# Performance work log

Measured on AMD Instinct MI355X. Metric: run time of the kernel, lower is better.

Reference implementation:

```python
import jax, jax.numpy as jnp
import numpy as np

H_SIZE = 2048
NUM_K_HEADS = 16
NUM_V_HEADS = 32
DK = 128
DV = 128
KEY_DIM = NUM_K_HEADS * DK        # 2048
VALUE_DIM = NUM_V_HEADS * DV      # 4096
CONV_DIM = 2 * KEY_DIM + VALUE_DIM  # 8192
KERNEL = 4
EPS = 1e-6
B, S = 2, 2048


def setup_inputs() -> dict:
    key = jax.random.key(0)
    ks = jax.random.split(key, 8)
    w = lambda k, shape, s: jax.random.normal(k, shape, jnp.float32) * s
    return {
        "hidden_states": jax.random.normal(ks[0], (B, S, H_SIZE), jnp.float32),
        "w_qkv": w(ks[1], (H_SIZE, CONV_DIM), 0.02),
        "w_z": w(ks[2], (H_SIZE, VALUE_DIM), 0.02),
        "w_b": w(ks[3], (H_SIZE, NUM_V_HEADS), 0.02),
        "w_a": w(ks[4], (H_SIZE, NUM_V_HEADS), 0.02),
        "conv_w": w(ks[5], (CONV_DIM, KERNEL), 0.2),
        "dt_bias": jnp.ones((NUM_V_HEADS,), jnp.float32),
        "A_log": jnp.zeros((NUM_V_HEADS,), jnp.float32),
        "norm_gamma": jnp.ones((DV,), jnp.float32),
        "w_out": w(ks[6], (VALUE_DIM, H_SIZE), 0.02),
    }


def _l2norm(x, eps=1e-6):
    return x * jax.lax.rsqrt(jnp.sum(x * x, axis=-1, keepdims=True) + eps)


def _causal_conv(x, w):
    # depthwise causal conv1d; x: (B,S,C), w: (C,K)
    K = w.shape[-1]
    Sq = x.shape[1]
    xp = jnp.pad(x, ((0, 0), (K - 1, 0), (0, 0)))
    out = xp[:, 0:Sq, :] * w[None, None, :, 0]
    for j in range(1, K):  # tiny fixed kernel loop (K=4)
        out = out + xp[:, j:j + Sq, :] * w[None, None, :, j]
    return out


def _forward(hidden_states, w_qkv, w_z, w_b, w_a, conv_w, dt_bias, A_log,
             norm_gamma, w_out):
    Bq, Sq, _ = hidden_states.shape
    mixed = hidden_states @ w_qkv                       # (B,S,CONV_DIM)
    z = (hidden_states @ w_z).reshape(Bq, Sq, NUM_V_HEADS, DV)
    b = hidden_states @ w_b                             # (B,S,Hv)
    a = hidden_states @ w_a                             # (B,S,Hv)
    mixed = jax.nn.silu(_causal_conv(mixed, conv_w))
    q, k, v = jnp.split(mixed, [KEY_DIM, 2 * KEY_DIM], axis=-1)
    q = q.reshape(Bq, Sq, NUM_K_HEADS, DK)
    k = k.reshape(Bq, Sq, NUM_K_HEADS, DK)
    v = v.reshape(Bq, Sq, NUM_V_HEADS, DV)
    nrep = NUM_V_HEADS // NUM_K_HEADS
    q = jnp.repeat(q, nrep, axis=2)                     # GQA expand -> Hv heads
    k = jnp.repeat(k, nrep, axis=2)
    beta = jax.nn.sigmoid(b)                            # write gate
    g = -jnp.exp(A_log)[None, None, :] * jax.nn.softplus(a + dt_bias[None, None, :])

    # gated delta rule recurrence in float32 (matches reference)
    qf = _l2norm(q.astype(jnp.float32)) * (DK ** -0.5)
    kf = _l2norm(k.astype(jnp.float32))
    vf = v.astype(jnp.float32)
    gf = g.astype(jnp.float32)
    bf = beta.astype(jnp.float32)

    def step(state, xs):
        q_t, k_t, v_t, g_t, b_t = xs  # (B,H,dk),(B,H,dk),(B,H,dv),(B,H),(B,H)
        state = state * jnp.exp(g_t)[..., None, None]
        kv = jnp.einsum('bhk,bhkv->bhv', k_t, state)
        delta = (v_t - kv) * b_t[..., None]
        state = state + jnp.einsum('bhk,bhv->bhkv', k_t, delta)
        out = jnp.einsum('bhk,bhkv->bhv', q_t, state)
        return state, out

    mv = lambda x: jnp.moveaxis(x, 1, 0)  # (B,S,...) -> (S,B,...)
    xs = (mv(qf), mv(kf), mv(vf), mv(gf), mv(bf))
    state0 = jnp.zeros((Bq, NUM_V_HEADS, DK, DV), jnp.float32)
    _, outs = jax.lax.scan(step, state0, xs)            # (S,B,H,dv)
    o = jnp.moveaxis(outs, 0, 1)                        # (B,S,H,dv)

    # gated RMSNorm over head_v_dim: gate with silu(z), then rms-normalize
    o = o * jax.nn.silu(z.astype(jnp.float32))
    o = o * jax.lax.rsqrt(jnp.mean(o * o, axis=-1, keepdims=True) + EPS)
    o = o * norm_gamma
    o = o.reshape(Bq, Sq, VALUE_DIM).astype(hidden_states.dtype)
    return o @ w_out


def reference(hidden_states, w_qkv, w_z, w_b, w_a, conv_w, dt_bias, A_log,
              norm_gamma, w_out):
    return _forward(hidden_states, w_qkv, w_z, w_b, w_a, conv_w, dt_bias,
                    A_log, norm_gamma, w_out)
```

## Files before the change

### kernel.cpp

```cpp
#include <hip/hip_runtime.h>
#include <hip/hip_bf16.h>
#include <cstdint>


#define HSZ 2048
#define NUM_K_HEADS 16
#define NUM_V_HEADS 32
#define DKH 128
#define DVH 128
#define KEY_DIM 2048
#define VALUE_DIM 4096
#define CONV_DIM 8192
#define BB 2
#define SSEQ 2048
#define MM (BB * SSEQ)
#define CHUNK 64
#define NCHUNK (SSEQ / CHUNK)
#define DVB 16

typedef __hip_bfloat16 bf16;
typedef short short8 __attribute__((ext_vector_type(8)));
typedef float f32x4 __attribute__((ext_vector_type(4)));

__device__ __forceinline__ float bfu(ushort u) {
  union { float f; uint32_t i; } x;
  x.i = ((uint32_t)u) << 16;
  return x.f;
}
__device__ __forceinline__ ushort f2b(float f) {
  bf16 h = __float2bfloat16(f);
  return *reinterpret_cast<ushort*>(&h);
}

__device__ __forceinline__ void gload16(const void* g, const void* l) {
  __builtin_amdgcn_global_load_lds(
      (const __attribute__((address_space(1))) unsigned int*)g,
      (__attribute__((address_space(3))) unsigned int*)(const_cast<void*>(l)),
      16, 0, 0);
}

__device__ __forceinline__ int kidx(int r, int d) {
  return r * 128 + (((d >> 3) ^ (r & 7)) << 3) + (d & 7);
}
__device__ __forceinline__ int widx(int r, int d) {
  return r * 64 + (((d >> 3) ^ (r & 7)) << 3) + (d & 7);
}

__global__ __launch_bounds__(256) void cast_bf16_kernel(
    const float* __restrict__ in, ushort* __restrict__ out, int n4) {
  int i = blockIdx.x * 256 + threadIdx.x;
  if (i < n4) {
    float4 v = ((const float4*)in)[i];
    ushort4 u;
    u.x = f2b(v.x); u.y = f2b(v.y); u.z = f2b(v.z); u.w = f2b(v.w);
    ((ushort4*)out)[i] = u;
  }
}

__global__ __launch_bounds__(256) void transpose_cast(
    const float* __restrict__ W, ushort* __restrict__ WT, int K, int N) {
  __shared__ ushort tile[32][33];
  const int tx = threadIdx.x & 31, ty = threadIdx.x >> 5;
  const int n0 = blockIdx.x * 32, k0 = blockIdx.y * 32;
#pragma unroll
  for (int i = 0; i < 4; ++i)
    tile[ty + i * 8][tx] = f2b(W[(size_t)(k0 + ty + i * 8) * N + n0 + tx]);
  __syncthreads();
#pragma unroll
  for (int i = 0; i < 4; ++i)
    WT[(size_t)(n0 + ty + i * 8) * K + k0 + tx] = tile[tx][ty + i * 8];
}

__global__ __launch_bounds__(512) void gemm256_fused(
    const ushort* __restrict__ A, const ushort* __restrict__ BT,
    ushort* __restrict__ Cm, ushort* __restrict__ Cz, int M, int K) {
  __shared__ __align__(16) ushort smem[256 * 264];
  const int t = threadIdx.x;
  const int w = t >> 6, lane = t & 63;
  const int m0 = blockIdx.y * 256, n0 = blockIdx.x * 256;
  const int wm = (w >> 2) * 128, wn = (w & 3) * 64;
  const int fr = lane & 15, kb = lane >> 4;
  const int srow = t >> 3;
  const int scol = (t & 7) * 8;
  const int ssw = ((scol >> 3) ^ (srow & 7)) << 3;
  const int rsw = fr & 7;
  f32x4 acc[8][4] = {};
  const int nt = K / 64;

#define STAGE_TILE(tt, buf)                                                   \
  {                                                                           \
    const int k0_ = (tt)*64;                                                  \
    ushort* As_ = smem + (buf)*32768;                                         \
    ushort* Bs_ = As_ + 16384;                                                \
    _Pragma("unroll") for (int p = 0; p < 4; ++p) {                           \
      const int row_ = p * 64 + srow;                                         \
      gload16(&A[(size_t)(m0 + row_) * K + k0_ + ssw],                        \
              &As_[row_ * 64 + scol]);                                        \
    }                                                                         \
    _Pragma("unroll") for (int p = 0; p < 4; ++p) {                           \
      const int row_ = p * 64 + srow;                                         \
      gload16(&BT[(size_t)(n0 + row_) * K + k0_ + ssw],                       \
              &Bs_[row_ * 64 + scol]);                                        \
    }                                                                         \
  }

  STAGE_TILE(0, 0);
  STAGE_TILE(1, 1);

  for (int tt = 0; tt < nt; ++tt) {
    const int buf = tt & 1;
    const ushort* As = smem + buf * 32768;
    const ushort* Bs = As + 16384;
    if (tt + 1 < nt)
      asm volatile("s_waitcnt vmcnt(8)" ::: "memory");
    else
      asm volatile("s_waitcnt vmcnt(0)" ::: "memory");
    __builtin_amdgcn_sched_barrier(0);
    __builtin_amdgcn_s_barrier();
    __builtin_amdgcn_sched_barrier(0);
#pragma unroll
    for (int ks = 0; ks < 2; ++ks) {
      const int kg = ks * 4 + kb;
      const int ca = ((kg ^ rsw) << 3);
      short8 af[8], bf_[4];
#pragma unroll
      for (int mf = 0; mf < 8; ++mf)
        af[mf] = *(const short8*)&As[(wm + mf * 16 + fr) * 64 + ca];
#pragma unroll
      for (int nf = 0; nf < 4; ++nf)
        bf_[nf] = *(const short8*)&Bs[(wn + nf * 16 + fr) * 64 + ca];
#pragma unroll
      for (int mf = 0; mf < 8; ++mf)
#pragma unroll
        for (int nf = 0; nf < 4; ++nf)
          acc[mf][nf] = __builtin_amdgcn_mfma_f32_16x16x32_bf16(
              af[mf], bf_[nf], acc[mf][nf], 0, 0, 0);
    }
    __builtin_amdgcn_sched_barrier(0);
    __builtin_amdgcn_s_barrier();
    __builtin_amdgcn_sched_barrier(0);
    if (tt + 2 < nt) STAGE_TILE(tt + 2, buf);
  }
#undef STAGE_TILE

  const int crow = wm + (lane >> 4) * 4;
  const int ccol = wn + fr;
#pragma unroll
  for (int mf = 0; mf < 8; ++mf)
#pragma unroll
    for (int nf = 0; nf < 4; ++nf)
#pragma unroll
      for (int j = 0; j < 4; ++j)
        smem[(crow + mf * 16 + j) * 264 + ccol + nf * 16] = f2b(acc[mf][nf][j]);
  __syncthreads();
  ushort* Cout = (n0 < CONV_DIM) ? Cm : Cz;
  const int Nout = (n0 < CONV_DIM) ? CONV_DIM : VALUE_DIM;
  const int ncol = (n0 < CONV_DIM) ? n0 : n0 - CONV_DIM;
#pragma unroll
  for (int p = 0; p < 16; ++p) {
    const int r = p * 16 + (t >> 5), cch = (t & 31) * 8;
    *(short8*)&Cout[(size_t)(m0 + r) * Nout + ncol + cch] =
        *(const short8*)&smem[r * 264 + cch];
  }
}

__global__ __launch_bounds__(256, 2) void gemm128_f32(
    const ushort* __restrict__ A, const ushort* __restrict__ BT,
    float* __restrict__ C, int M, int N, int K) {
  __shared__ __align__(16) ushort smem[2 * 16384];
  const int t = threadIdx.x;
  const int w = t >> 6, lane = t & 63;
  const int m0 = blockIdx.y * 128, n0 = blockIdx.x * 128;
  const int wm = (w >> 1) * 64, wn = (w & 1) * 64;
  const int fr = lane & 15, kb = lane >> 4;
  const int srow = t >> 3;
  const int scol = (t & 7) * 8;
  const int ssw = ((scol >> 3) ^ (srow & 7)) << 3;
  const int rsw = fr & 7;
  f32x4 acc[4][4] = {};
  const int nt = K / 64;

#define STAGE128(tt, buf)                                                     \
  {                                                                           \
    const int k0_ = (tt)*64;                                                  \
    ushort* As_ = smem + (buf)*16384;                                         \
    ushort* Bs_ = As_ + 8192;                                                 \
    _Pragma("unroll") for (int p = 0; p < 4; ++p) {                           \
      const int row_ = p * 32 + srow;                                         \
      gload16(&A[(size_t)(m0 + row_) * K + k0_ + ssw],                        \
              &As_[row_ * 64 + scol]);                                        \
    }                                                                         \
    _Pragma("unroll") for (int p = 0; p < 4; ++p) {                           \
      const int row_ = p * 32 + srow;                                         \
      gload16(&BT[(size_t)(n0 + row_) * K + k0_ + ssw],                       \
              &Bs_[row_ * 64 + scol]);                                        \
    }                                                                         \
  }

  STAGE128(0, 0);
  STAGE128(1, 1);

  for (int tt = 0; tt < nt; ++tt) {
    const int buf = tt & 1;
    const ushort* As = smem + buf * 16384;
    const ushort* Bs = As + 8192;
    if (tt + 1 < nt)
      asm volatile("s_waitcnt vmcnt(8)" ::: "memory");
    else
      asm volatile("s_waitcnt vmcnt(0)" ::: "memory");
    __builtin_amdgcn_sched_barrier(0);
    __builtin_amdgcn_s_barrier();
    __builtin_amdgcn_sched_barrier(0);
#pragma unroll
    for (int ks = 0; ks < 2; ++ks) {
      const int kg = ks * 4 + kb;
      const int ca = ((kg ^ rsw) << 3);
      short8 af[4], bfr[4];
#pragma unroll
      for (int mf = 0; mf < 4; ++mf)
        af[mf] = *(const short8*)&As[(wm + mf * 16 + fr) * 64 + ca];
#pragma unroll
      for (int nf = 0; nf < 4; ++nf)
        bfr[nf] = *(const short8*)&Bs[(wn + nf * 16 + fr) * 64 + ca];
#pragma unroll
      for (int mf = 0; mf < 4; ++mf)
#pragma unroll
        for (int nf = 0; nf < 4; ++nf)
          acc[mf][nf] = __builtin_amdgcn_mfma_f32_16x16x32_bf16(
              af[mf], bfr[nf], acc[mf][nf], 0, 0, 0);
    }
    __builtin_amdgcn_sched_barrier(0);
    __builtin_amdgcn_s_barrier();
    __builtin_amdgcn_sched_barrier(0);
    if (tt + 2 < nt) STAGE128(tt + 2, buf);
  }
#undef STAGE128

  const int orow = m0 + wm + (lane >> 4) * 4;
  const int ocol = n0 + wn + fr;
#pragma unroll
  for (int mf = 0; mf < 4; ++mf)
#pragma unroll
    for (int nf = 0; nf < 4; ++nf)
#pragma unroll
      for (int j = 0; j < 4; ++j)
        C[(size_t)(orow + mf * 16 + j) * N + ocol + nf * 16] = acc[mf][nf][j];
}

__global__ __launch_bounds__(256) void ba_kernel(
    const float* __restrict__ hs, const float* __restrict__ w_b,
    const float* __restrict__ w_a, const float* __restrict__ dt_bias,
    const float* __restrict__ A_log, float* __restrict__ gbuf,
    float* __restrict__ beta) {
  const int row0 = blockIdx.x * 8;
  const int t = threadIdx.x;
  __shared__ float hsr[8][HSZ];
  __shared__ float red[2][256];
  {
    const float4* src = (const float4*)(hs + (size_t)row0 * HSZ);
    for (int i = t; i < 8 * HSZ / 4; i += 256) ((float4*)hsr)[i] = src[i];
  }
  __syncthreads();
  const int h = t & 31, p = t >> 5;
  float sb[8] = {}, sa[8] = {};
  const int kbeg = p * 256;
  for (int k = kbeg; k < kbeg + 256; ++k) {
    float wb = w_b[k * NUM_V_HEADS + h];
    float wa = w_a[k * NUM_V_HEADS + h];
#pragma unroll
    for (int r = 0; r < 8; ++r) {
      float x = hsr[r][k];
      sb[r] += x * wb;
      sa[r] += x * wa;
    }
  }
#pragma unroll
  for (int r = 0; r < 8; ++r) {
    red[0][t] = sb[r];
    red[1][t] = sa[r];
    __syncthreads();
    if (t < NUM_V_HEADS) {
      float b = 0.f, a = 0.f;
#pragma unroll
      for (int q = 0; q < 8; ++q) {
        b += red[0][t + 32 * q];
        a += red[1][t + 32 * q];
      }
      float bet = 1.f / (1.f + expf(-b));
      float x = a + dt_bias[t];
      float sp = (x > 20.f) ? x : log1pf(expf(x));
      gbuf[(size_t)(row0 + r) * NUM_V_HEADS + t] = -expf(A_log[t]) * sp;
      beta[(size_t)(row0 + r) * NUM_V_HEADS + t] = bet;
    }
    __syncthreads();
  }
}

__global__ __launch_bounds__(256) void conv_kernel(
    const ushort* __restrict__ mixed, const float* __restrict__ conv_w,
    ushort* __restrict__ qkv) {
  const int bid = blockIdx.x;
  const int slice = bid & 3;
  const int row0 = (bid >> 2) * 8;
  const int s0 = row0 & (SSEQ - 1);
  const int t = threadIdx.x;
  const int cbase = slice * 2048 + t * 8;

  float wreg[4][8];
#pragma unroll
  for (int e = 0; e < 8; ++e) {
    float4 wv = *(const float4*)&conv_w[(cbase + e) * 4];
    wreg[0][e] = wv.x;
    wreg[1][e] = wv.y;
    wreg[2][e] = wv.z;
    wreg[3][e] = wv.w;
  }

  const ushort* mp = mixed + (size_t)row0 * CONV_DIM + cbase;
  short8 win[4];
  const short8 z8 = {0, 0, 0, 0, 0, 0, 0, 0};
#pragma unroll
  for (int j = 0; j < 3; ++j)
    win[j] = (s0 - 3 + j >= 0) ? *(const short8*)&mp[(ptrdiff_t)(j - 3) * CONV_DIM]
                               : z8;

  if (slice < 2) {
    float vals[8][8];
    float ssq[8];
#pragma unroll
    for (int r = 0; r < 8; ++r) {
      win[3] = *(const short8*)&mp[(ptrdiff_t)r * CONV_DIM];
      float sq = 0.f;
#pragma unroll
      for (int e = 0; e < 8; ++e) {
        float a = bfu((ushort)win[0][e]) * wreg[0][e] +
                  bfu((ushort)win[1][e]) * wreg[1][e] +
                  bfu((ushort)win[2][e]) * wreg[2][e] +
                  bfu((ushort)win[3][e]) * wreg[3][e];
        float x = a / (1.f + expf(-a));
        vals[r][e] = x;
        sq += x * x;
      }
      ssq[r] = sq;
      win[0] = win[1];
      win[1] = win[2];
      win[2] = win[3];
    }
#pragma unroll
    for (int r = 0; r < 8; ++r) {
      float sq = ssq[r];
      sq += __shfl_xor(sq, 1, 64);
      sq += __shfl_xor(sq, 2, 64);
      sq += __shfl_xor(sq, 4, 64);
      sq += __shfl_xor(sq, 8, 64);
      float sc = rsqrtf(sq + 1e-6f);
      if (slice == 0) sc *= 0.08838834764831845f;
      short8 o;
#pragma unroll
      for (int e = 0; e < 8; ++e) o[e] = (short)f2b(vals[r][e] * sc);
      *(short8*)&qkv[(size_t)(row0 + r) * CONV_DIM + cbase] = o;
    }
  } else {
#pragma unroll
    for (int r = 0; r < 8; ++r) {
      win[3] = *(const short8*)&mp[(ptrdiff_t)r * CONV_DIM];
      short8 o;
#pragma unroll
      for (int e = 0; e < 8; ++e) {
        float a = bfu((ushort)win[0][e]) * wreg[0][e] +
                  bfu((ushort)win[1][e]) * wreg[1][e] +
                  bfu((ushort)win[2][e]) * wreg[2][e] +
                  bfu((ushort)win[3][e]) * wreg[3][e];
        o[e] = (short)f2b(a / (1.f + expf(-a)));
      }
      *(short8*)&qkv[(size_t)(row0 + r) * CONV_DIM + cbase] = o;
      win[0] = win[1];
      win[1] = win[2];
      win[2] = win[3];
    }
  }
}

__global__ __launch_bounds__(256) void chunk_T_kernel(
    const ushort* __restrict__ qkv, const float* __restrict__ gbuf,
    const float* __restrict__ beta, ushort* __restrict__ Tbuf,
    ushort* __restrict__ Wbuf) {
  const int bid = blockIdx.x;
  const int c = bid & 31;
  const int h = (bid >> 5) & 31;
  const int b = bid >> 10;
  const int hk = h >> 1;
  const int t = threadIdx.x;
  const int w = t >> 6, lane = t & 63;
  const int fr = lane & 15, fq = lane >> 4;

  __shared__ ushort Klds[64 * 128];
  __shared__ ushort Qlds[64 * 128];
  __shared__ __align__(16) float AT[64][68];
  __shared__ ushort Wlds[64 * 64];
  __shared__ float Gs[64], Bsh[64];

  const int row0 = b * SSEQ + c * CHUNK;
  const int qcol = hk * DKH;
  const int kcol = KEY_DIM + hk * DKH;

#pragma unroll
  for (int r = 0; r < 4; ++r) {
    int vi = t + 256 * r;
    int row = vi >> 4, gr = vi & 15;
    const size_t gb = (size_t)(row0 + row) * CONV_DIM;
    *(short8*)&Klds[row * 128 + ((gr ^ (row & 7)) << 3)] =
        *(const short8*)&qkv[gb + kcol + gr * 8];
    *(short8*)&Qlds[row * 128 + ((gr ^ (row & 7)) << 3)] =
        *(const short8*)&qkv[gb + qcol + gr * 8];
  }
  if (t < 64) {
    float s = gbuf[(size_t)(row0 + t) * NUM_V_HEADS + h];
#pragma unroll
    for (int off = 1; off < 64; off <<= 1) {
      float p = __shfl_up(s, off, 64);
      if (lane >= off) s += p;
    }
    Gs[t] = s;
    Bsh[t] = beta[(size_t)(row0 + t) * NUM_V_HEADS + h];
  }
  __syncthreads();

  f32x4 kkt[4] = {}, qkt[4] = {};
#pragma unroll
  for (int ks = 0; ks < 4; ++ks) {
    int d0 = ks * 32 + fq * 8;
    short8 xk = *(const short8*)&Klds[kidx(w * 16 + fr, d0)];
    short8 xq = *(const short8*)&Qlds[kidx(w * 16 + fr, d0)];
#pragma unroll
    for (int j = 0; j < 4; ++j) {
      short8 yk = *(const short8*)&Klds[kidx(j * 16 + fr, d0)];
      kkt[j] = __builtin_amdgcn_mfma_f32_16x16x32_bf16(xk, yk, kkt[j], 0, 0, 0);
      qkt[j] = __builtin_amdgcn_mfma_f32_16x16x32_bf16(xq, yk, qkt[j], 0, 0, 0);
    }
  }
#pragma unroll
  for (int j = 0; j < 4; ++j)
#pragma unroll
    for (int jj = 0; jj < 4; ++jj) {
      int i = w * 16 + fq * 4 + jj;
      int jc = j * 16 + fr;
      AT[jc][i] = (jc < i) ? Bsh[i] * __expf(Gs[i] - Gs[jc]) * kkt[j][jj] : 0.f;
      float val = (jc <= i) ? __expf(Gs[i] - Gs[jc]) * qkt[j][jj] : 0.f;
      Wlds[widx(i, jc)] = f2b(val);
    }
  __syncthreads();

  {
    ushort* Wg = Wbuf + (size_t)bid * 4096;
#pragma unroll
    for (int e = 0; e < 8; ++e)
      ((uint*)Wg)[e * 256 + t] = ((const uint*)Wlds)[e * 256 + t];
  }

  if (w == 0) {
    float u[64];
#pragma unroll
    for (int i = 0; i < 64; ++i) u[i] = (i == lane) ? 1.f : 0.f;
#pragma unroll
    for (int j = 0; j < 63; ++j) {
      float xj = u[j];
      const int i0 = (j + 1) & ~3;
#pragma unroll
      for (int ii = i0; ii < 64; ii += 4) {
        float4 a4 = *(const float4*)&AT[j][ii];
        if (ii + 0 > j) u[ii + 0] -= a4.x * xj;
        if (ii + 1 > j) u[ii + 1] -= a4.y * xj;
        if (ii + 2 > j) u[ii + 2] -= a4.z * xj;
        if (ii + 3 > j) u[ii + 3] -= a4.w * xj;
      }
    }
    ushort* Tg = Tbuf + (size_t)bid * 4096;
#pragma unroll
    for (int i = 0; i < 64; ++i) Tg[i * 64 + lane] = f2b(u[i]);
  }
}

__global__ __launch_bounds__(256, 2) void recur_chunk_kernel(
    const ushort* __restrict__ qkv, const float* __restrict__ gbuf,
    const float* __restrict__ beta, const ushort* __restrict__ Tbuf,
    const ushort* __restrict__ Wbuf, float* __restrict__ o) {
  const int bid = blockIdx.x;
  const int dvq = bid & 7;
  const int h = (bid >> 3) & 31;
  const int b = bid >> 8;
  const int hk = h >> 1;
  const int t = threadIdx.x;
  const int w = t >> 6, lane = t & 63;
  const int fr = lane & 15, fq = lane >> 4;

  __shared__ ushort Klds[64 * 128];
  __shared__ ushort Vlds[64 * DVB];
  __shared__ ushort Sth[DVB * 128];
  __shared__ ushort Stl[DVB * 128];
  __shared__ ushort Th[64 * 64];
  __shared__ ushort Wlds[64 * 64];
  __shared__ ushort Ut[DVB * 64];
  __shared__ ushort UTs[DVB * 64];
  __shared__ ushort UTo[DVB * 64];
  __shared__ float Gs[64], Bsh[64];

  float sreg[2][4] = {};

  const int qcol = hk * DKH;
  const int kcol = KEY_DIM + hk * DKH;
  const int vcol = 2 * KEY_DIM + h * DVH + dvq * DVB;
  const int ocol = h * DVH + dvq * DVB;
  const size_t tbase0 = ((size_t)(b * 32 + h) * 32) * 4096;

  short8 pK[4], pT0, pT1, pV, pxq[4];
  uint pW[8];
  float pg = 0.f, pb = 0.f;

  auto prefetch = [&](int c) {
    const int row0 = b * SSEQ + c * CHUNK;
#pragma unroll
    for (int ks = 0; ks < 4; ++ks)
      pxq[ks] = *(const short8*)&qkv[(size_t)(row0 + w * 16 + fr) * CONV_DIM +
                                     qcol + ks * 32 + fq * 8];
    const ushort* Tg = Tbuf + tbase0 + (size_t)c * 4096;
    const ushort* Wg = Wbuf + tbase0 + (size_t)c * 4096;
    pT0 = *(const short8*)&Tg[t * 16];
    pT1 = *(const short8*)&Tg[t * 16 + 8];
#pragma unroll
    for (int e = 0; e < 8; ++e) pW[e] = ((const uint*)Wg)[e * 256 + t];
#pragma unroll
    for (int r = 0; r < 4; ++r) {
      int vi = t + 256 * r;
      int row = vi >> 4, gr = vi & 15;
      pK[r] = *(const short8*)&qkv[(size_t)(row0 + row) * CONV_DIM + kcol + gr * 8];
    }
    if (t < 128) {
      int row = t >> 1, c0 = (t & 1) * 8;
      pV = *(const short8*)&qkv[(size_t)(row0 + row) * CONV_DIM + vcol + c0];
    }
    if (t < 64) {
      pg = gbuf[(size_t)(row0 + t) * NUM_V_HEADS + h];
      pb = beta[(size_t)(row0 + t) * NUM_V_HEADS + h];
    }
  };

  prefetch(0);

  for (int c = 0; c < NCHUNK; ++c) {
    const int row0 = b * SSEQ + c * CHUNK;

    short8 xq[4];
#pragma unroll
    for (int ks = 0; ks < 4; ++ks) xq[ks] = pxq[ks];
#pragma unroll
    for (int e = 0; e < 8; ++e) ((uint*)Wlds)[e * 256 + t] = pW[e];
#pragma unroll
    for (int r = 0; r < 4; ++r) {
      int vi = t + 256 * r;
      int row = vi >> 4, gr = vi & 15;
      *(short8*)&Klds[row * 128 + ((gr ^ (row & 7)) << 3)] = pK[r];
    }
    if (t < 128) {
      int row = t >> 1, c0 = (t & 1) * 8;
      *(short8*)&Vlds[row * DVB + c0] = pV;
    }
    if (t < 64) {
      float s = pg;
#pragma unroll
      for (int off = 1; off < 64; off <<= 1) {
        float p = __shfl_up(s, off, 64);
        if (lane >= off) s += p;
      }
      Gs[t] = s;
      Bsh[t] = pb;
    }
#pragma unroll
    for (int dt = 0; dt < 2; ++dt)
#pragma unroll
      for (int jj = 0; jj < 4; ++jj) {
        int d = (w * 2 + dt) * 16 + fq * 4 + jj;
        float f = sreg[dt][jj];
        ushort hi = f2b(f);
        int idx = kidx(fr, d);
        Sth[idx] = hi;
        Stl[idx] = f2b(f - bfu(hi));
      }
    {
      int r = t >> 2, d0 = (t & 3) * 16;
      *(short8*)&Th[widx(r, d0)] = pT0;
      *(short8*)&Th[widx(r, d0 + 8)] = pT1;
    }
    __syncthreads();

    if (c + 1 < NCHUNK) prefetch(c + 1);

    f32x4 ks0 = {}, qs0 = {};
#pragma unroll
    for (int ks = 0; ks < 4; ++ks) {
      int d0 = ks * 32 + fq * 8;
      short8 xk = *(const short8*)&Klds[kidx(w * 16 + fr, d0)];
      short8 yh = *(const short8*)&Sth[kidx(fr, d0)];
      short8 yl = *(const short8*)&Stl[kidx(fr, d0)];
      ks0 = __builtin_amdgcn_mfma_f32_16x16x32_bf16(xk, yh, ks0, 0, 0, 0);
      ks0 = __builtin_amdgcn_mfma_f32_16x16x32_bf16(xk, yl, ks0, 0, 0, 0);
      qs0 = __builtin_amdgcn_mfma_f32_16x16x32_bf16(xq[ks], yh, qs0, 0, 0, 0);
      qs0 = __builtin_amdgcn_mfma_f32_16x16x32_bf16(xq[ks], yl, qs0, 0, 0, 0);
    }
    f32x4 oacc;
#pragma unroll
    for (int jj = 0; jj < 4; ++jj) {
      int i = w * 16 + fq * 4 + jj;
      float eg = __expf(Gs[i]);
      float rhs = Bsh[i] * (bfu(Vlds[i * DVB + fr]) - eg * ks0[jj]);
      Ut[widx(fr, i)] = f2b(rhs);
      oacc[jj] = qs0[jj] * eg;
    }
    __syncthreads();

    {
      f32x4 uacc = {};
#pragma unroll
      for (int ks = 0; ks < 2; ++ks) {
        int j0 = ks * 32 + fq * 8;
        short8 ta = *(const short8*)&Th[widx(w * 16 + fr, j0)];
        short8 ub = *(const short8*)&Ut[widx(fr, j0)];
        uacc = __builtin_amdgcn_mfma_f32_16x16x32_bf16(ta, ub, uacc, 0, 0, 0);
      }
#pragma unroll
      for (int jj = 0; jj < 4; ++jj) {
        int i = w * 16 + fq * 4 + jj;
        float u = uacc[jj];
        UTo[widx(fr, i)] = f2b(u);
        UTs[widx(fr, i)] = f2b(u * __expf(Gs[63] - Gs[i]));
      }
    }
    __syncthreads();

#pragma unroll
    for (int ks = 0; ks < 2; ++ks) {
      int i0 = ks * 32 + fq * 8;
      short8 xw = *(const short8*)&Wlds[widx(w * 16 + fr, i0)];
      short8 yu = *(const short8*)&UTo[widx(fr, i0)];
      oacc = __builtin_amdgcn_mfma_f32_16x16x32_bf16(xw, yu, oacc, 0, 0, 0);
    }
#pragma unroll
    for (int jj = 0; jj < 4; ++jj) {
      int tt = w * 16 + fq * 4 + jj;
      o[(size_t)(row0 + tt) * VALUE_DIM + ocol + fr] = oacc[jj];
    }
    {
      float eGC = __expf(Gs[63]);
#pragma unroll
      for (int dt = 0; dt < 2; ++dt) {
        const int dk0 = (w * 2 + dt) * 16;
        f32x4 sacc;
#pragma unroll
        for (int jj = 0; jj < 4; ++jj) sacc[jj] = sreg[dt][jj] * eGC;
        const int dkr = dk0 + fr;
#pragma unroll
        for (int ks = 0; ks < 2; ++ks) {
          short8 xk;
#pragma unroll
          for (int e = 0; e < 8; ++e)
            xk[e] = (short)Klds[kidx(ks * 32 + fq * 8 + e, dkr)];
          short8 yu = *(const short8*)&UTs[widx(fr, ks * 32 + fq * 8)];
          sacc = __builtin_amdgcn_mfma_f32_16x16x32_bf16(xk, yu, sacc, 0, 0, 0);
        }
#pragma unroll
        for (int jj = 0; jj < 4; ++jj) sreg[dt][jj] = sacc[jj];
      }
    }
    __syncthreads();
  }
}

__global__ __launch_bounds__(256) void gnorm_kernel(
    const float* __restrict__ o, const ushort* __restrict__ z,
    const float* __restrict__ gamma, ushort* __restrict__ ob) {
  const int row = blockIdx.x;
  const int t = threadIdx.x;
  const int grp = t >> 3, r = t & 7;
  const float* op = o + (size_t)row * VALUE_DIM + grp * DVH + r * 16;
  const ushort* zp = z + (size_t)row * VALUE_DIM + grp * DVH + r * 16;
  ushort* obp = ob + (size_t)row * VALUE_DIM + grp * DVH + r * 16;
  float4 ov[4];
  short8 zv[2];
#pragma unroll
  for (int q = 0; q < 4; ++q) ov[q] = *(const float4*)&op[q * 4];
  zv[0] = *(const short8*)&zp[0];
  zv[1] = *(const short8*)&zp[8];
  float vals[16];
  float ssq = 0.f;
#pragma unroll
  for (int i = 0; i < 16; ++i) {
    float zz = bfu((ushort)zv[i >> 3][i & 7]);
    float oo = ((const float*)&ov[i >> 2])[i & 3];
    float x = oo * (zz / (1.f + expf(-zz)));
    vals[i] = x;
    ssq += x * x;
  }
  ssq += __shfl_xor(ssq, 1, 64);
  ssq += __shfl_xor(ssq, 2, 64);
  ssq += __shfl_xor(ssq, 4, 64);
  float sc = rsqrtf(ssq * (1.f / 128.f) + 1e-6f);
  short8 o0, o1;
#pragma unroll
  for (int i = 0; i < 8; ++i) {
    o0[i] = (short)f2b(vals[i] * sc * gamma[r * 16 + i]);
    o1[i] = (short)f2b(vals[8 + i] * sc * gamma[r * 16 + 8 + i]);
  }
  *(short8*)&obp[0] = o0;
  *(short8*)&obp[8] = o1;
}

extern "C" void kernel_launch(void* const* d_in, const int* in_sizes, int n_in,
                              void* d_out, int out_size, void* d_ws,
                              size_t ws_size, hipStream_t stream) {
  const float* hs = (const float*)d_in[0];
  const float* w_qkv = (const float*)d_in[1];
  const float* w_z = (const float*)d_in[2];
  const float* w_b = (const float*)d_in[3];
  const float* w_a = (const float*)d_in[4];
  const float* conv_w = (const float*)d_in[5];
  const float* dt_bias = (const float*)d_in[6];
  const float* A_log = (const float*)d_in[7];
  const float* gamma = (const float*)d_in[8];
  const float* w_out = (const float*)d_in[9];
  float* out = (float*)d_out;
  char* wsb = (char*)d_ws;

  ushort* hs_b = (ushort*)wsb;
  ushort* wqkvT = hs_b + (size_t)MM * HSZ;
  ushort* wzT = wqkvT + (size_t)CONV_DIM * HSZ;
  ushort* woutT = wzT + (size_t)VALUE_DIM * HSZ;
  ushort* mixed = woutT + (size_t)HSZ * VALUE_DIM;
  ushort* qkv = mixed + (size_t)MM * CONV_DIM;
  ushort* z = qkv + (size_t)MM * CONV_DIM;
  float* gbuf = (float*)(z + (size_t)MM * VALUE_DIM);
  float* beta = gbuf + (size_t)MM * NUM_V_HEADS;
  float* o = (float*)mixed;
  ushort* ob = qkv;
  ushort* Tbuf = hs_b;
  ushort* Wbuf = wqkvT;

  cast_bf16_kernel<<<(MM * HSZ / 4 + 255) / 256, 256, 0, stream>>>(
      hs, hs_b, MM * HSZ / 4);
  transpose_cast<<<dim3(CONV_DIM / 32, HSZ / 32), 256, 0, stream>>>(
      w_qkv, wqkvT, HSZ, CONV_DIM);
  transpose_cast<<<dim3(VALUE_DIM / 32, HSZ / 32), 256, 0, stream>>>(
      w_z, wzT, HSZ, VALUE_DIM);
  transpose_cast<<<dim3(HSZ / 32, VALUE_DIM / 32), 256, 0, stream>>>(
      w_out, woutT, VALUE_DIM, HSZ);

  gemm256_fused<<<dim3((CONV_DIM + VALUE_DIM) / 256, MM / 256), 512, 0,
                  stream>>>(hs_b, wqkvT, mixed, z, MM, HSZ);
  ba_kernel<<<MM / 8, 256, 0, stream>>>(hs, w_b, w_a, dt_bias, A_log, gbuf,
                                        beta);
  conv_kernel<<<2048, 256, 0, stream>>>(mixed, conv_w, qkv);
  chunk_T_kernel<<<2048, 256, 0, stream>>>(qkv, gbuf, beta, Tbuf, Wbuf);
  recur_chunk_kernel<<<512, 256, 0, stream>>>(qkv, gbuf, beta, Tbuf, Wbuf, o);
  gnorm_kernel<<<MM, 256, 0, stream>>>(o, z, gamma, ob);
  gemm128_f32<<<dim3(HSZ / 128, MM / 128), 256, 0, stream>>>(
      ob, woutT, out, MM, HSZ, VALUE_DIM);
}
```

Baseline: 687.4 us.

## Use four-buffer K=32 pipeline with single barrier per iteration in GEMMs

Both GEMM kernels switch from double-buffered 64-wide K tiles to four rotating 32-wide K buffers in the same shared memory footprint. The prefetch for tile tt+2 is issued right after the top barrier, so the trailing barrier per iteration is dropped. The LDS swizzle is redone for 32-element rows. This trades one barrier per 64 K for one per 32 K and fewer MFMAs per sync, while aiming for better overlap of loads with compute.

```diff
diff --git a/kernel.cpp b/kernel.cpp
--- a/kernel.cpp
+++ b/kernel.cpp
@@ -80,69 +80,65 @@
   const int m0 = blockIdx.y * 256, n0 = blockIdx.x * 256;
   const int wm = (w >> 2) * 128, wn = (w & 3) * 64;
   const int fr = lane & 15, kb = lane >> 4;
-  const int srow = t >> 3;
-  const int scol = (t & 7) * 8;
-  const int ssw = ((scol >> 3) ^ (srow & 7)) << 3;
-  const int rsw = fr & 7;
+  const int srow = t >> 2;
+  const int sg = t & 3;
+  const int ssw = ((sg ^ ((srow >> 1) & 3)) << 3);
   f32x4 acc[8][4] = {};
-  const int nt = K / 64;
-
-#define STAGE_TILE(tt, buf)                                                   \
+  const int nt = K / 32;
+
+#define STAGE_F(tt, buf)                                                      \
   {                                                                           \
-    const int k0_ = (tt)*64;                                                  \
-    ushort* As_ = smem + (buf)*32768;                                         \
-    ushort* Bs_ = As_ + 16384;                                                \
-    _Pragma("unroll") for (int p = 0; p < 4; ++p) {                           \
-      const int row_ = p * 64 + srow;                                         \
+    const int k0_ = (tt)*32;                                                  \
+    ushort* As_ = smem + (buf)*16384;                                         \
+    ushort* Bs_ = As_ + 8192;                                                 \
+    _Pragma("unroll") for (int p = 0; p < 2; ++p) {                           \
+      const int row_ = p * 128 + srow;                                        \
       gload16(&A[(size_t)(m0 + row_) * K + k0_ + ssw],                        \
-              &As_[row_ * 64 + scol]);                                        \
+              &As_[row_ * 32 + sg * 8]);                                      \
     }                                                                         \
-    _Pragma("unroll") for (int p = 0; p < 4; ++p) {                           \
-      const int row_ = p * 64 + srow;                                         \
+    _Pragma("unroll") for (int p = 0; p < 2; ++p) {                           \
+      const int row_ = p * 128 + srow;                                        \
       gload16(&BT[(size_t)(n0 + row_) * K + k0_ + ssw],                       \
-              &Bs_[row_ * 64 + scol]);                                        \
+              &Bs_[row_ * 32 + sg * 8]);                                      \
     }                                                                         \
   }
 
-  STAGE_TILE(0, 0);
-  STAGE_TILE(1, 1);
+  STAGE_F(0, 0);
+  STAGE_F(1, 1);
 
   for (int tt = 0; tt < nt; ++tt) {
-    const int buf = tt & 1;
-    const ushort* As = smem + buf * 32768;
-    const ushort* Bs = As + 16384;
+    const int buf = tt & 3;
     if (tt + 1 < nt)
-      asm volatile("s_waitcnt vmcnt(8)" ::: "memory");
+      asm volatile("s_waitcnt vmcnt(4)" ::: "memory");
     else
       asm volatile("s_waitcnt vmcnt(0)" ::: "memory");
     __builtin_amdgcn_sched_barrier(0);
     __builtin_amdgcn_s_barrier();
     __builtin_amdgcn_sched_barrier(0);
-#pragma unroll
-    for (int ks = 0; ks < 2; ++ks) {
-      const int kg = ks * 4 + kb;
-      const int ca = ((kg ^ rsw) << 3);
-      short8 af[8], bf_[4];
-#pragma unroll
-      for (int mf = 0; mf < 8; ++mf)
-        af[mf] = *(const short8*)&As[(wm + mf * 16 + fr) * 64 + ca];
+    if (tt + 2 < nt) STAGE_F(tt + 2, (tt + 2) & 3);
+    const ushort* As = smem + buf * 16384;
+    const ushort* Bs = As + 8192;
+    short8 af[8], bf_[4];
+#pragma unroll
+    for (int nf = 0; nf < 4; ++nf) {
+      const int row = wn + nf * 16 + fr;
+      bf_[nf] = *(const short8*)&Bs[row * 32 + ((kb ^ ((row >> 1) & 3)) << 3)];
+    }
+#pragma unroll
+    for (int mf = 0; mf < 8; ++mf) {
+      const int row = wm + mf * 16 + fr;
+      af[mf] = *(const short8*)&As[row * 32 + ((kb ^ ((row >> 1) & 3)) << 3)];
+    }
+#pragma unroll
+    for (int mf = 0; mf < 8; ++mf)
 #pragma unroll
       for (int nf = 0; nf < 4; ++nf)
-        bf_[nf] = *(const short8*)&Bs[(wn + nf * 16 + fr) * 64 + ca];
-#pragma unroll
-      for (int mf = 0; mf < 8; ++mf)
-#pragma unroll
-        for (int nf = 0; nf < 4; ++nf)
-          acc[mf][nf] = __builtin_amdgcn_mfma_f32_16x16x32_bf16(
-              af[mf], bf_[nf], acc[mf][nf], 0, 0, 0);
-    }
-    __builtin_amdgcn_sched_barrier(0);
-    __builtin_amdgcn_s_barrier();
-    __builtin_amdgcn_sched_barrier(0);
-    if (tt + 2 < nt) STAGE_TILE(tt + 2, buf);
-  }
-#undef STAGE_TILE
-
+        acc[mf][nf] = __builtin_amdgcn_mfma_f32_16x16x32_bf16(
+            af[mf], bf_[nf], acc[mf][nf], 0, 0, 0);
+  }
+#undef STAGE_F
+
+  __syncthreads();
   const int crow = wm + (lane >> 4) * 4;
   const int ccol = wn + fr;
 #pragma unroll
@@ -167,74 +163,69 @@
 __global__ __launch_bounds__(256, 2) void gemm128_f32(
     const ushort* __restrict__ A, const ushort* __restrict__ BT,
     float* __restrict__ C, int M, int N, int K) {
-  __shared__ __align__(16) ushort smem[2 * 16384];
+  __shared__ __align__(16) ushort smem[4 * 8192];
   const int t = threadIdx.x;
   const int w = t >> 6, lane = t & 63;
   const int m0 = blockIdx.y * 128, n0 = blockIdx.x * 128;
   const int wm = (w >> 1) * 64, wn = (w & 1) * 64;
   const int fr = lane & 15, kb = lane >> 4;
-  const int srow = t >> 3;
-  const int scol = (t & 7) * 8;
-  const int ssw = ((scol >> 3) ^ (srow & 7)) << 3;
-  const int rsw = fr & 7;
+  const int srow = t >> 2;
+  const int sg = t & 3;
+  const int ssw = ((sg ^ ((srow >> 1) & 3)) << 3);
   f32x4 acc[4][4] = {};
-  const int nt = K / 64;
-
-#define STAGE128(tt, buf)                                                     \
+  const int nt = K / 32;
+
+#define STAGE_G(tt, buf)                                                      \
   {                                                                           \
-    const int k0_ = (tt)*64;                                                  \
-    ushort* As_ = smem + (buf)*16384;                                         \
-    ushort* Bs_ = As_ + 8192;                                                 \
-    _Pragma("unroll") for (int p = 0; p < 4; ++p) {                           \
-      const int row_ = p * 32 + srow;                                         \
+    const int k0_ = (tt)*32;                                                  \
+    ushort* As_ = smem + (buf)*8192;                                          \
+    ushort* Bs_ = As_ + 4096;                                                 \
+    _Pragma("unroll") for (int p = 0; p < 2; ++p) {                           \
+      const int row_ = p * 64 + srow;                                         \
       gload16(&A[(size_t)(m0 + row_) * K + k0_ + ssw],                        \
-              &As_[row_ * 64 + scol]);                                        \
+              &As_[row_ * 32 + sg * 8]);                                      \
     }                                                                         \
-    _Pragma("unroll") for (int p = 0; p < 4; ++p) {                           \
-      const int row_ = p * 32 + srow;                                         \
+    _Pragma("unroll") for (int p = 0; p < 2; ++p) {                           \
+      const int row_ = p * 64 + srow;                                         \
       gload16(&BT[(size_t)(n0 + row_) * K + k0_ + ssw],                       \
-              &Bs_[row_ * 64 + scol]);                                        \
+              &Bs_[row_ * 32 + sg * 8]);                                      \
     }                                                                         \
   }
 
-  STAGE128(0, 0);
-  STAGE128(1, 1);
+  STAGE_G(0, 0);
+  STAGE_G(1, 1);
 
   for (int tt = 0; tt < nt; ++tt) {
-    const int buf = tt & 1;
-    const ushort* As = smem + buf * 16384;
-    const ushort* Bs = As + 8192;
+    const int buf = tt & 3;
     if (tt + 1 < nt)
-      asm volatile("s_waitcnt vmcnt(8)" ::: "memory");
+      asm volatile("s_waitcnt vmcnt(4)" ::: "memory");
     else
       asm volatile("s_waitcnt vmcnt(0)" ::: "memory");
     __builtin_amdgcn_sched_barrier(0);
     __builtin_amdgcn_s_barrier();
     __builtin_amdgcn_sched_barrier(0);
-#pragma unroll
-    for (int ks = 0; ks < 2; ++ks) {
-      const int kg = ks * 4 + kb;
-      const int ca = ((kg ^ rsw) << 3);
-      short8 af[4], bfr[4];
-#pragma unroll
-      for (int mf = 0; mf < 4; ++mf)
-        af[mf] = *(const short8*)&As[(wm + mf * 16 + fr) * 64 + ca];
+    if (tt + 2 < nt) STAGE_G(tt + 2, (tt + 2) & 3);
+    const ushort* As = smem + buf * 8192;
+    const ushort* Bs = As + 4096;
+    short8 af[4], bfr[4];
+#pragma unroll
+    for (int nf = 0; nf < 4; ++nf) {
+      const int row = wn + nf * 16 + fr;
+      bfr[nf] = *(const short8*)&Bs[row * 32 + ((kb ^ ((row >> 1) & 3)) << 3)];
+    }
+#pragma unroll
+    for (int mf = 0; mf < 4; ++mf) {
+      const int row = wm + mf * 16 + fr;
+      af[mf] = *(const short8*)&As[row * 32 + ((kb ^ ((row >> 1) & 3)) << 3)];
+    }
+#pragma unroll
+    for (int mf = 0; mf < 4; ++mf)
 #pragma unroll
       for (int nf = 0; nf < 4; ++nf)
-        bfr[nf] = *(const short8*)&Bs[(wn + nf * 16 + fr) * 64 + ca];
-#pragma unroll
-      for (int mf = 0; mf < 4; ++mf)
-#pragma unroll
-        for (int nf = 0; nf < 4; ++nf)
-          acc[mf][nf] = __builtin_amdgcn_mfma_f32_16x16x32_bf16(
-              af[mf], bfr[nf], acc[mf][nf], 0, 0, 0);
-    }
-    __builtin_amdgcn_sched_barrier(0);
-    __builtin_amdgcn_s_barrier();
-    __builtin_amdgcn_sched_barrier(0);
-    if (tt + 2 < nt) STAGE128(tt + 2, buf);
-  }
-#undef STAGE128
+        acc[mf][nf] = __builtin_amdgcn_mfma_f32_16x16x32_bf16(
+            af[mf], bfr[nf], acc[mf][nf], 0, 0, 0);
+  }
+#undef STAGE_G
 
   const int orow = m0 + wm + (lane >> 4) * 4;
   const int ocol = n0 + wn + fr;
```

Result: no change. 699.4 us (+1.7%).
